# Performance work log

Measured on AMD Instinct MI355X. Metric: run time of the kernel, lower is better.

## Reference

```python
import jax, jax.numpy as jnp
import numpy as np

N = 60000      # total nodes
D = 300        # feature dim
R = 5          # num relations == num bases
E = 1_000_000  # edges
S = 25000      # last_idx_senses
G = 50000      # last_idx_globals
BATCH = 32


def setup_inputs() -> dict:
    key = jax.random.key(0)
    ks = jax.random.split(key, 12)
    x = jax.random.normal(ks[0], (N, D), dtype=jnp.float32)
    edge_index = jax.random.randint(ks[1], (2, E), 0, N, dtype=jnp.int32)
    edge_type = jax.random.randint(ks[2], (E,), 0, R, dtype=jnp.int32)
    current_node_index = jax.random.randint(ks[3], (BATCH,), 0, N, dtype=jnp.int32)
    scale = 1.0 / np.sqrt(D)
    # RGCNConv basis decomposition params (num_bases == num_relations)
    basis = jax.random.normal(ks[4], (R, D, D), dtype=jnp.float32) * scale
    comp = jax.random.normal(ks[5], (R, R), dtype=jnp.float32) * scale
    root = jax.random.normal(ks[6], (D, D), dtype=jnp.float32) * scale
    bias = jnp.zeros((D,), dtype=jnp.float32)
    # heads
    w_global = jax.random.normal(ks[7], (G - S, D), dtype=jnp.float32) * scale
    b_global = jnp.zeros((G - S,), dtype=jnp.float32)
    w_sense = jax.random.normal(ks[8], (S, D), dtype=jnp.float32) * scale
    b_sense = jnp.zeros((S,), dtype=jnp.float32)
    return {
        "x": x, "edge_index": edge_index, "edge_type": edge_type,
        "current_node_index": current_node_index,
        "basis": basis, "comp": comp, "root": root, "bias": bias,
        "w_global": w_global, "b_global": b_global,
        "w_sense": w_sense, "b_sense": b_sense,
    }


def reference(x, edge_index, edge_type, current_node_index,
              basis, comp, root, bias,
              w_global, b_global, w_sense, b_sense):
    src, dst = edge_index[0], edge_index[1]
    # Combined segment id over (dst node, relation): mean-aggregate source
    # features per (node, relation), then apply the per-relation transform
    # (mean(x_j) @ W_r == mean(x_j @ W_r); matches PyG RGCNConv aggr='mean').
    seg = dst * R + edge_type                      # [E]
    msg_sum = jax.ops.segment_sum(x[src], seg, num_segments=N * R)  # [N*R, D]
    cnt = jax.ops.segment_sum(jnp.ones((E,), jnp.float32), seg, num_segments=N * R)
    mean = msg_sum.reshape(N, R, D) / jnp.maximum(cnt.reshape(N, R, 1), 1.0)
    # basis decomposition: W_r = sum_b comp[r,b] * basis[b]
    W = jnp.einsum('rb,bij->rij', comp, basis)     # [R, D, D]
    agg = jnp.einsum('nrd,rde->ne', mean, W)       # [N, D]
    h = jax.nn.relu(agg + x @ root + bias)         # [N, D]
    hc = h[current_node_index]                     # [B, D]
    logits_global = hc @ w_global.T + b_global     # [B, G-S]
    logits_sense = hc @ w_sense.T + b_sense        # [B, S]
    return (jax.nn.log_softmax(logits_global, axis=-1),
            jax.nn.log_softmax(logits_sense, axis=-1))
```

## Files before the change

kernel.cpp:

```cpp
#include <hip/hip_runtime.h>
#include <hip/hip_bf16.h>
#include <math.h>

#define D 300
#define R 5
#define NE 1000000
#define B 32
#define NG 25000
#define NS 25000
#define NROWS 50000
#define NT16 3125
#define HST 324

typedef __bf16 bf16x8 __attribute__((ext_vector_type(8)));
typedef float f32x4 __attribute__((ext_vector_type(4)));


__device__ __forceinline__ void online_upd(float& m, float& s, float v) {
    if (v > m) { s = s * __expf(m - v) + 1.0f; m = v; }
    else       { s += __expf(v - m); }
}
__device__ __forceinline__ void online_merge(float& m, float& s, float om, float os) {
    float M = fmaxf(m, om);
    s = s * __expf(m - M) + os * __expf(om - M);
    m = M;
}

__global__ void zero_ws(float4* __restrict__ p) {
    int i = blockIdx.x * 256 + threadIdx.x;
    if (i < 14440) p[i] = float4{0.f, 0.f, 0.f, 0.f};
}

__global__ __launch_bounds__(256) void scan_accum(
        const int* __restrict__ ei, const int* __restrict__ et,
        const int* __restrict__ cur, const float* __restrict__ x,
        float* __restrict__ wsum, float* __restrict__ wcnt) {
    __shared__ unsigned int tbl[32];
    __shared__ int curl[B];
    __shared__ int lcnt;
    __shared__ int2 loc[64];
    int tid = threadIdx.x;
    if (tid < 32) tbl[tid] = 0u;
    if (tid == 0) lcnt = 0;
    __syncthreads();
    if (tid < B) { int c = cur[tid]; curl[tid] = c; atomicOr(&tbl[(c >> 5) & 31], 1u << (c & 31)); }
    __syncthreads();
    long base = ((long)blockIdx.x * 256 + tid) * 4;
    if (base < NE) {
        int ds4[4];
        if (base + 4 <= NE) {
            int4 d4 = *(const int4*)(ei + NE + base);
            ds4[0] = d4.x; ds4[1] = d4.y; ds4[2] = d4.z; ds4[3] = d4.w;
        } else {
            for (int k = 0; k < 4; ++k) ds4[k] = (base + k < NE) ? ei[NE + base + k] : -1;
        }
        #pragma unroll
        for (int k = 0; k < 4; ++k) {
            int dst = ds4[k];
            if (dst < 0) continue;
            if (!(tbl[(dst >> 5) & 31] & (1u << (dst & 31)))) continue;
            int e = (int)base + k;
            int r = -1, src = 0;
            for (int b = 0; b < B; ++b) {
                if (dst == curl[b]) {
                    if (r < 0) { r = et[e]; src = ei[e]; }
                    atomicAdd(&wcnt[b * R + r], 1.0f);
                    int p = atomicAdd(&lcnt, 1);
                    if (p < 64) loc[p] = int2{src, b * R + r};
                }
            }
        }
    }
    __syncthreads();
    int n = lcnt; if (n > 64) n = 64;
    for (int m = 0; m < n; ++m) {
        int2 pr = loc[m];
        const float* xs = x + (long)pr.x * D;
        float* sm = wsum + (long)pr.y * D;
        for (int t = tid; t < D; t += 256) atomicAdd(&sm[t], xs[t]);
    }
}

__global__ __launch_bounds__(320) void rgcn_hc(
        const float* __restrict__ x, const int* __restrict__ cur,
        const float* __restrict__ comp, const float* __restrict__ root,
        const float* __restrict__ basis, const float* __restrict__ wsum,
        const float* __restrict__ wcnt, float* __restrict__ hcf) {
    int kc = blockIdx.x, t = threadIdx.x;
    __shared__ float uL[800];
    __shared__ float inv[B * R];
    __shared__ float cmp[R * R];
    if (t < B * R) inv[t] = 1.0f / fmaxf(wcnt[t], 1.0f);
    if (t >= 160 && t < 160 + R * R) cmp[t - 160] = comp[t - 160];
    __syncthreads();
    int d0 = kc * 25;
    if (d0 < 300) {
        for (int i = t; i < 800; i += 320) {
            int b = i / 25, dd = i - b * 25;
            uL[i] = x[(long)cur[b] * D + d0 + dd];
        }
    } else {
        int g0 = d0 - 300;
        int bb = g0 / 300, t0 = g0 - bb * 300;
        for (int i = t; i < 800; i += 320) {
            int b = i / 25, dd = i - b * 25;
            float a = 0.f;
            #pragma unroll
            for (int r = 0; r < R; ++r)
                a = fmaf(cmp[r * R + bb] * inv[b * R + r], wsum[(long)(b * R + r) * D + t0 + dd], a);
            uL[i] = a;
        }
    }
    __syncthreads();
    if (t < D) {
        const float* Mb = (d0 < 300) ? (root + (long)d0 * D) : (basis + (long)(d0 - 300) * D);
        float acc[B] = {};
        #pragma unroll 5
        for (int i = 0; i < 25; ++i) {
            float m = Mb[(long)i * D + t];
            #pragma unroll
            for (int b = 0; b < B; ++b) acc[b] = fmaf(uL[b * 25 + i], m, acc[b]);
        }
        for (int b = 0; b < B; ++b) atomicAdd(&hcf[b * D + t], acc[b]);
    }
}

__global__ __launch_bounds__(256) void head_gemm(
    const float* __restrict__ hcf, const float* __restrict__ bias,
    const float* __restrict__ wg, const float* __restrict__ bg,
    const float* __restrict__ wsn, const float* __restrict__ bsn,
    float* __restrict__ out, float2* __restrict__ pm2) {
    __shared__ __bf16 hcbL[32 * HST];
    int tid = threadIdx.x;
    for (int i = tid; i < 32 * HST; i += 256) {
        int b = i / HST, kk = i - b * HST;
        float v = 0.f;
        if (kk < D) v = fmaxf(hcf[b * D + kk] + bias[kk], 0.f);
        hcbL[i] = (__bf16)v;
    }
    __syncthreads();

    int wid = tid >> 6, l = tid & 63, ln = l & 15, og = l >> 4;
    int jt = blockIdx.x * 4 + wid;
    if (jt >= NT16) return;
    int j0 = jt * 16;
    int row = j0 + ln;
    const float* wrow = ((row < NG) ? (wg + (long)row * D) : (wsn + (long)(row - NG) * D)) + og * 8;

    float4 w[20];
    #pragma unroll
    for (int s = 0; s < 9; ++s) {
        w[2 * s]     = *(const float4*)(wrow + 32 * s);
        w[2 * s + 1] = *(const float4*)(wrow + 32 * s + 4);
    }
    {
        w[18] = float4{0.f, 0.f, 0.f, 0.f};
        w[19] = float4{0.f, 0.f, 0.f, 0.f};
        if (og == 0) { w[18] = *(const float4*)(wrow + 288); w[19] = *(const float4*)(wrow + 292); }
        else if (og == 1) { w[18] = *(const float4*)(wrow + 288); }
    }
    __builtin_amdgcn_sched_barrier(0);

    const __bf16* hrow0 = hcbL + ln * HST + og * 8;
    const __bf16* hrow1 = hcbL + (16 + ln) * HST + og * 8;
    f32x4 acc0 = {}, acc1 = {};
    #pragma unroll
    for (int s = 0; s < 10; ++s) {
        float4 w0 = w[2 * s], w1 = w[2 * s + 1];
        bf16x8 a;
        a[0]=(__bf16)w0.x; a[1]=(__bf16)w0.y; a[2]=(__bf16)w0.z; a[3]=(__bf16)w0.w;
        a[4]=(__bf16)w1.x; a[5]=(__bf16)w1.y; a[6]=(__bf16)w1.z; a[7]=(__bf16)w1.w;
        acc0 = __builtin_amdgcn_mfma_f32_16x16x32_bf16(a, *(const bf16x8*)(hrow0 + 32 * s), acc0, 0, 0, 0);
        acc1 = __builtin_amdgcn_mfma_f32_16x16x32_bf16(a, *(const bf16x8*)(hrow1 + 32 * s), acc1, 0, 0, 0);
    }

    int b0 = ln, b1 = 16 + ln;
    float m0 = -3.0e38f, s0 = 0.f, m1 = -3.0e38f, s1 = 0.f;
    float m2 = -3.0e38f, s2 = 0.f, m3 = -3.0e38f, s3 = 0.f;
    #pragma unroll
    for (int r = 0; r < 4; ++r) {
        int j = j0 + og * 4 + r;
        float bv = (j < NG) ? bg[j] : bsn[j - NG];
        float v0 = acc0[r] + bv;
        float v1 = acc1[r] + bv;
        float* op0 = (j < NG) ? (out + (long)b0 * NG + j)
                              : (out + (long)B * NG + (long)b0 * NS + (j - NG));
        float* op1 = (j < NG) ? (out + (long)b1 * NG + j)
                              : (out + (long)B * NG + (long)b1 * NS + (j - NG));
        *op0 = v0;
        *op1 = v1;
        if (j < NG) { online_upd(m0, s0, v0); online_upd(m2, s2, v1); }
        else        { online_upd(m1, s1, v0); online_upd(m3, s3, v1); }
    }
    #pragma unroll
    for (int o = 16; o <= 32; o <<= 1) {
        float tm, ts;
        tm = __shfl_xor(m0, o); ts = __shfl_xor(s0, o); online_merge(m0, s0, tm, ts);
        tm = __shfl_xor(m1, o); ts = __shfl_xor(s1, o); online_merge(m1, s1, tm, ts);
        tm = __shfl_xor(m2, o); ts = __shfl_xor(s2, o); online_merge(m2, s2, tm, ts);
        tm = __shfl_xor(m3, o); ts = __shfl_xor(s3, o); online_merge(m3, s3, tm, ts);
    }
    if (og == 0) {
        pm2[(long)b0 * NT16 + jt]       = float2{m0, s0};
        pm2[(long)(B + b0) * NT16 + jt] = float2{m1, s1};
        pm2[(long)b1 * NT16 + jt]       = float2{m2, s2};
        pm2[(long)(B + b1) * NT16 + jt] = float2{m3, s3};
    }
}

__global__ __launch_bounds__(256) void lse_sub(float* __restrict__ out,
                                               const float2* __restrict__ pm2) {
    int rw = blockIdx.x / 25, c = blockIdx.x % 25;
    int tid = threadIdx.x;
    const float2* pr = pm2 + (long)rw * NT16;
    float m = -3.0e38f, s = 0.f;
    for (int i = tid; i < NT16; i += 256) { float2 e = pr[i]; online_merge(m, s, e.x, e.y); }
    #pragma unroll
    for (int o = 32; o; o >>= 1) {
        float om = __shfl_xor(m, o), os = __shfl_xor(s, o);
        online_merge(m, s, om, os);
    }
    __shared__ float sm[4], ss[4];
    __shared__ float lseS;
    if ((tid & 63) == 0) { sm[tid >> 6] = m; ss[tid >> 6] = s; }
    __syncthreads();
    if (tid == 0) {
        float M = sm[0], S = ss[0];
        for (int w = 1; w < 4; ++w) online_merge(M, S, sm[w], ss[w]);
        lseS = M + __logf(S);
    }
    __syncthreads();
    float l = lseS;
    float4* o4 = (float4*)out + (long)rw * 6250 + c * 250;
    if (tid < 250) { float4 v = o4[tid]; v.x -= l; v.y -= l; v.z -= l; v.w -= l; o4[tid] = v; }
}

extern "C" void kernel_launch(void* const* d_in, const int* in_sizes, int n_in,
                              void* d_out, int out_size, void* d_ws, size_t ws_size,
                              hipStream_t stream) {
    const float* x     = (const float*)d_in[0];
    const int*   ei    = (const int*)d_in[1];
    const int*   et    = (const int*)d_in[2];
    const int*   cur   = (const int*)d_in[3];
    const float* basis = (const float*)d_in[4];
    const float* comp  = (const float*)d_in[5];
    const float* root  = (const float*)d_in[6];
    const float* bias  = (const float*)d_in[7];
    const float* wg    = (const float*)d_in[8];
    const float* bgl   = (const float*)d_in[9];
    const float* wsn   = (const float*)d_in[10];
    const float* bsn   = (const float*)d_in[11];
    float* out  = (float*)d_out;
    float* wsf  = (float*)d_ws;
    float*  wsum = wsf;
    float*  wcnt = wsf + 48000;
    float*  hcf  = wsf + 48160;
    float2* pm2  = (float2*)(wsf + 57760);

    zero_ws<<<57, 256, 0, stream>>>((float4*)d_ws);
    scan_accum<<<977, 256, 0, stream>>>(ei, et, cur, x, wsum, wcnt);
    rgcn_hc<<<72, 320, 0, stream>>>(x, cur, comp, root, basis, wsum, wcnt, hcf);
    head_gemm<<<(NT16 + 3) / 4, 256, 0, stream>>>(hcf, bias, wg, bgl, wsn, bsn, out, pm2);
    lse_sub<<<1600, 256, 0, stream>>>(out, pm2);
}
```

Baseline: 74.70 us.

## Remap head_gemm blocks per XCD and reduce softmax partials per block

Blocks of head_gemm are remapped so that each XCD handles a contiguous range of weight rows, which is meant to improve L2 locality. The per-wave log-sum-exp partials are now merged in shared memory, so each block writes one partial instead of four. That cuts pm2 traffic and the work lse_sub spends reducing it. The fully preloaded weight registers and the sched_barrier are dropped in favour of loads inside the loop. This lowers register pressure but may expose more load latency, and the new __syncthreads makes out-of-range waves stay in the block instead of exiting early.

```diff
diff --git a/kernel.cpp b/kernel.cpp
--- a/kernel.cpp
+++ b/kernel.cpp
@@ -10,6 +10,9 @@
 #define NS 25000
 #define NROWS 50000
 #define NT16 3125
+#define NBLK2 782
+#define XQ 97
+#define XR 6
 #define HST 324
 
 typedef __bf16 bf16x8 __attribute__((ext_vector_type(8)));
@@ -131,6 +134,7 @@
     const float* __restrict__ wsn, const float* __restrict__ bsn,
     float* __restrict__ out, float2* __restrict__ pm2) {
     __shared__ __bf16 hcbL[32 * HST];
+    __shared__ float2 sred[4][4][16];
     int tid = threadIdx.x;
     for (int i = tid; i < 32 * HST; i += 256) {
         int b = i / HST, kk = i - b * HST;
@@ -140,57 +144,61 @@
     }
     __syncthreads();
 
+    int orig = blockIdx.x;
+    int xcd = orig & 7, off = orig >> 3;
+    int wgid = (xcd < XR ? xcd * (XQ + 1) : XR * (XQ + 1) + (xcd - XR) * XQ) + off;
+
     int wid = tid >> 6, l = tid & 63, ln = l & 15, og = l >> 4;
-    int jt = blockIdx.x * 4 + wid;
-    if (jt >= NT16) return;
-    int j0 = jt * 16;
-    int row = j0 + ln;
+    int jt = wgid * 4 + wid;
+    bool valid = jt < NT16;
+    int jtc = valid ? jt : NT16 - 1;
+    int jw = jtc * 16;
+    int row = jw + ln;
     const float* wrow = ((row < NG) ? (wg + (long)row * D) : (wsn + (long)(row - NG) * D)) + og * 8;
-
-    float4 w[20];
-    #pragma unroll
-    for (int s = 0; s < 9; ++s) {
-        w[2 * s]     = *(const float4*)(wrow + 32 * s);
-        w[2 * s + 1] = *(const float4*)(wrow + 32 * s + 4);
-    }
-    {
-        w[18] = float4{0.f, 0.f, 0.f, 0.f};
-        w[19] = float4{0.f, 0.f, 0.f, 0.f};
-        if (og == 0) { w[18] = *(const float4*)(wrow + 288); w[19] = *(const float4*)(wrow + 292); }
-        else if (og == 1) { w[18] = *(const float4*)(wrow + 288); }
-    }
-    __builtin_amdgcn_sched_barrier(0);
 
     const __bf16* hrow0 = hcbL + ln * HST + og * 8;
     const __bf16* hrow1 = hcbL + (16 + ln) * HST + og * 8;
     f32x4 acc0 = {}, acc1 = {};
     #pragma unroll
-    for (int s = 0; s < 10; ++s) {
-        float4 w0 = w[2 * s], w1 = w[2 * s + 1];
+    for (int s = 0; s < 9; ++s) {
+        float4 w0 = *(const float4*)(wrow + 32 * s);
+        float4 w1 = *(const float4*)(wrow + 32 * s + 4);
         bf16x8 a;
         a[0]=(__bf16)w0.x; a[1]=(__bf16)w0.y; a[2]=(__bf16)w0.z; a[3]=(__bf16)w0.w;
         a[4]=(__bf16)w1.x; a[5]=(__bf16)w1.y; a[6]=(__bf16)w1.z; a[7]=(__bf16)w1.w;
         acc0 = __builtin_amdgcn_mfma_f32_16x16x32_bf16(a, *(const bf16x8*)(hrow0 + 32 * s), acc0, 0, 0, 0);
         acc1 = __builtin_amdgcn_mfma_f32_16x16x32_bf16(a, *(const bf16x8*)(hrow1 + 32 * s), acc1, 0, 0, 0);
     }
+    {
+        float4 w0 = float4{0.f,0.f,0.f,0.f}, w1 = float4{0.f,0.f,0.f,0.f};
+        if (og == 0) { w0 = *(const float4*)(wrow + 288); w1 = *(const float4*)(wrow + 292); }
+        else if (og == 1) { w0 = *(const float4*)(wrow + 288); }
+        bf16x8 a;
+        a[0]=(__bf16)w0.x; a[1]=(__bf16)w0.y; a[2]=(__bf16)w0.z; a[3]=(__bf16)w0.w;
+        a[4]=(__bf16)w1.x; a[5]=(__bf16)w1.y; a[6]=(__bf16)w1.z; a[7]=(__bf16)w1.w;
+        acc0 = __builtin_amdgcn_mfma_f32_16x16x32_bf16(a, *(const bf16x8*)(hrow0 + 288), acc0, 0, 0, 0);
+        acc1 = __builtin_amdgcn_mfma_f32_16x16x32_bf16(a, *(const bf16x8*)(hrow1 + 288), acc1, 0, 0, 0);
+    }
 
     int b0 = ln, b1 = 16 + ln;
     float m0 = -3.0e38f, s0 = 0.f, m1 = -3.0e38f, s1 = 0.f;
     float m2 = -3.0e38f, s2 = 0.f, m3 = -3.0e38f, s3 = 0.f;
-    #pragma unroll
-    for (int r = 0; r < 4; ++r) {
-        int j = j0 + og * 4 + r;
-        float bv = (j < NG) ? bg[j] : bsn[j - NG];
-        float v0 = acc0[r] + bv;
-        float v1 = acc1[r] + bv;
-        float* op0 = (j < NG) ? (out + (long)b0 * NG + j)
-                              : (out + (long)B * NG + (long)b0 * NS + (j - NG));
-        float* op1 = (j < NG) ? (out + (long)b1 * NG + j)
-                              : (out + (long)B * NG + (long)b1 * NS + (j - NG));
-        *op0 = v0;
-        *op1 = v1;
-        if (j < NG) { online_upd(m0, s0, v0); online_upd(m2, s2, v1); }
-        else        { online_upd(m1, s1, v0); online_upd(m3, s3, v1); }
+    if (valid) {
+        #pragma unroll
+        for (int r = 0; r < 4; ++r) {
+            int j = jw + og * 4 + r;
+            float bv = (j < NG) ? bg[j] : bsn[j - NG];
+            float v0 = acc0[r] + bv;
+            float v1 = acc1[r] + bv;
+            float* op0 = (j < NG) ? (out + (long)b0 * NG + j)
+                                  : (out + (long)B * NG + (long)b0 * NS + (j - NG));
+            float* op1 = (j < NG) ? (out + (long)b1 * NG + j)
+                                  : (out + (long)B * NG + (long)b1 * NS + (j - NG));
+            *op0 = v0;
+            *op1 = v1;
+            if (j < NG) { online_upd(m0, s0, v0); online_upd(m2, s2, v1); }
+            else        { online_upd(m1, s1, v0); online_upd(m3, s3, v1); }
+        }
     }
     #pragma unroll
     for (int o = 16; o <= 32; o <<= 1) {
@@ -200,11 +208,20 @@
         tm = __shfl_xor(m2, o); ts = __shfl_xor(s2, o); online_merge(m2, s2, tm, ts);
         tm = __shfl_xor(m3, o); ts = __shfl_xor(s3, o); online_merge(m3, s3, tm, ts);
     }
-    if (og == 0) {
-        pm2[(long)b0 * NT16 + jt]       = float2{m0, s0};
-        pm2[(long)(B + b0) * NT16 + jt] = float2{m1, s1};
-        pm2[(long)b1 * NT16 + jt]       = float2{m2, s2};
-        pm2[(long)(B + b1) * NT16 + jt] = float2{m3, s3};
+    if (l < 16) {
+        sred[wid][0][ln] = float2{m0, s0};
+        sred[wid][1][ln] = float2{m1, s1};
+        sred[wid][2][ln] = float2{m2, s2};
+        sred[wid][3][ln] = float2{m3, s3};
+    }
+    __syncthreads();
+    if (tid < 64) {
+        int k = tid >> 4, lnn = tid & 15;
+        float m = -3.0e38f, s = 0.f;
+        #pragma unroll
+        for (int w = 0; w < 4; ++w) online_merge(m, s, sred[w][k][lnn].x, sred[w][k][lnn].y);
+        int rw = (k & 1) * 32 + (k >> 1) * 16 + lnn;
+        pm2[(long)rw * NBLK2 + wgid] = float2{m, s};
     }
 }
 
@@ -212,9 +229,9 @@
                                                const float2* __restrict__ pm2) {
     int rw = blockIdx.x / 25, c = blockIdx.x % 25;
     int tid = threadIdx.x;
-    const float2* pr = pm2 + (long)rw * NT16;
+    const float2* pr = pm2 + (long)rw * NBLK2;
     float m = -3.0e38f, s = 0.f;
-    for (int i = tid; i < NT16; i += 256) { float2 e = pr[i]; online_merge(m, s, e.x, e.y); }
+    for (int i = tid; i < NBLK2; i += 256) { float2 e = pr[i]; online_merge(m, s, e.x, e.y); }
     #pragma unroll
     for (int o = 32; o; o >>= 1) {
         float om = __shfl_xor(m, o), os = __shfl_xor(s, o);
@@ -260,6 +277,6 @@
     zero_ws<<<57, 256, 0, stream>>>((float4*)d_ws);
     scan_accum<<<977, 256, 0, stream>>>(ei, et, cur, x, wsum, wcnt);
     rgcn_hc<<<72, 320, 0, stream>>>(x, cur, comp, root, basis, wsum, wcnt, hcf);
-    head_gemm<<<(NT16 + 3) / 4, 256, 0, stream>>>(hcf, bias, wg, bgl, wsn, bsn, out, pm2);
+    head_gemm<<<NBLK2, 256, 0, stream>>>(hcf, bias, wg, bgl, wsn, bsn, out, pm2);
     lse_sub<<<1600, 256, 0, stream>>>(out, pm2);
 }
```

Result: faster. 71.39 us (median of 2 runs) (-4.4%).
